# Kernel optimization log

Hardware: AMD Instinct MI355X
Metric: run time of the kernel (lower is better)

## Reference

```python
import jax, jax.numpy as jnp
import numpy as np

D_MODEL = 512
NUM_HEADS = 8
HEAD_DIM = D_MODEL // NUM_HEADS


def setup_inputs() -> dict:
    key = jax.random.key(0)
    ks = jax.random.split(key, 12)
    B, S, D = 4, 2048, D_MODEL
    s = 1.0 / np.sqrt(D)
    return {
        "x": jax.random.normal(ks[0], (B, S, D), dtype=jnp.float32),
        "timestamps": jax.random.uniform(ks[1], (B, S), dtype=jnp.float32),
        "attention_mask": jnp.ones((B, S), dtype=jnp.int32),
        "Wq": jax.random.normal(ks[2], (D, D), dtype=jnp.float32) * s,
        "bq": jnp.zeros((D,), dtype=jnp.float32),
        "Wk": jax.random.normal(ks[3], (D, D), dtype=jnp.float32) * s,
        "bk": jnp.zeros((D,), dtype=jnp.float32),
        "Wv": jax.random.normal(ks[4], (D, D), dtype=jnp.float32) * s,
        "bv": jnp.zeros((D,), dtype=jnp.float32),
        "Wo": jax.random.normal(ks[5], (D, D), dtype=jnp.float32) * s,
        "bo": jnp.zeros((D,), dtype=jnp.float32),
        "decay_lambda": jnp.ones((NUM_HEADS,), dtype=jnp.float32),
    }


def reference(x, timestamps, attention_mask, Wq, bq, Wk, bk, Wv, bv, Wo, bo, decay_lambda):
    B, S, D = x.shape
    H, hd = NUM_HEADS, HEAD_DIM
    scale = hd ** -0.5
    q = (x @ Wq + bq).reshape(B, S, H, hd)
    k = (x @ Wk + bk).reshape(B, S, H, hd)
    v = (x @ Wv + bv).reshape(B, S, H, hd)
    # [B,H,S,S] raw scores
    scores = jnp.einsum("bihd,bjhd->bhij", q, k) * scale
    # learnable exponential time decay, multiplied into scores
    time_diff_abs = jnp.abs(timestamps[:, :, None] - timestamps[:, None, :])  # [B,S,S]
    lam = jax.nn.softplus(decay_lambda)  # [H]
    decay_bias = jnp.exp(-lam[None, :, None, None] * time_diff_abs[:, None])  # [B,H,S,S]
    scores = scores * decay_bias
    # mask over key positions
    scores = jnp.where(attention_mask[:, None, None, :] == 0, -jnp.inf, scores)
    attn = jax.nn.softmax(scores, axis=-1)
    out = jnp.einsum("bhij,bjhd->bihd", attn, v).reshape(B, S, D)
    out = out @ Wo + bo
    return out, attn
```

## Files before the change

kernel.cpp:

```cpp
#include <hip/hip_runtime.h>


#define S_LEN  2048
#define DM     512
#define NH     8
#define HDIM   64
#define BATCH  4
#define BHN    32
#define BSROWS 8192

typedef __attribute__((ext_vector_type(8))) short short8v;
typedef __attribute__((ext_vector_type(8))) unsigned short ushort8v;
typedef __attribute__((ext_vector_type(4))) unsigned short ushort4v;
typedef __attribute__((ext_vector_type(4))) float f32x4;
typedef __attribute__((ext_vector_type(2))) unsigned int uint2v;

static __device__ __forceinline__ unsigned short bf16_rne(float f){
  unsigned int u = __float_as_uint(f);
  u = (u + 0x7FFFu + ((u >> 16) & 1u)) >> 16;
  return (unsigned short)u;
}
static __device__ __forceinline__ float bf16_f32(unsigned short h){
  return __uint_as_float(((unsigned int)h) << 16);
}
static __device__ __forceinline__ unsigned int pack2bf(float a, float b){
  return (unsigned int)bf16_rne(a) | ((unsigned int)bf16_rne(b) << 16);
}
static __device__ __forceinline__ f32x4 mfma16(short8v a, short8v b, f32x4 c){
  return __builtin_amdgcn_mfma_f32_16x16x32_bf16(a, b, c, 0, 0, 0);
}
static __device__ __forceinline__ void gll16(const unsigned short* g, unsigned short* l){
  __builtin_amdgcn_global_load_lds(
      (const __attribute__((address_space(1))) unsigned int*)g,
      (__attribute__((address_space(3))) unsigned int*)l, 16, 0, 0);
}

__global__ void k_split(const float* __restrict__ src,
                        unsigned short* __restrict__ hi,
                        unsigned short* __restrict__ lo, int n){
  for (int i = blockIdx.x*blockDim.x + threadIdx.x; i < n;
       i += gridDim.x*blockDim.x){
    float f = src[i];
    unsigned short h = bf16_rne(f);
    hi[i] = h;
    lo[i] = bf16_rne(f - bf16_f32(h));
  }
}

__global__ void k_wsplit4(
    const float* __restrict__ Wq, const float* __restrict__ Wk,
    const float* __restrict__ Wv, const float* __restrict__ Wo,
    unsigned short* __restrict__ qkvh, unsigned short* __restrict__ qkvl,
    unsigned short* __restrict__ oh,   unsigned short* __restrict__ ol)
{
  int idx = blockIdx.x*blockDim.x + threadIdx.x;
  int wsel = idx >> 18;
  int off  = idx & 262143;
  int n = off >> 9, k = off & 511;
  const float* W = wsel==0 ? Wq : wsel==1 ? Wk : wsel==2 ? Wv : Wo;
  unsigned short* H = (wsel<3) ? (qkvh + (size_t)wsel*262144) : oh;
  unsigned short* L = (wsel<3) ? (qkvl + (size_t)wsel*262144) : ol;
  float f = W[k*DM + n];
  unsigned short h = bf16_rne(f);
  H[off] = h;
  L[off] = bf16_rne(f - bf16_f32(h));
}

__global__ __launch_bounds__(256, 3) void k_gemm_qkv(
    const unsigned short* __restrict__ Ahi, const unsigned short* __restrict__ Alo,
    const unsigned short* __restrict__ BThi, const unsigned short* __restrict__ BTlo,
    const float* __restrict__ bq, const float* __restrict__ bk,
    const float* __restrict__ bv,
    unsigned short* __restrict__ qhi, unsigned short* __restrict__ qlo,
    unsigned short* __restrict__ khi, unsigned short* __restrict__ klo,
    unsigned short* __restrict__ vt)
{
  const int K = DM;
  __shared__ __align__(16) unsigned short At[2][2][128][32];
  __shared__ __align__(16) unsigned short Bt[2][2][64][32];
  const int lane = threadIdx.x & 63, w = threadIdx.x >> 6;
  const int lr = lane & 15, lk = lane >> 4;
  const int rowbase = blockIdx.y*128;
  const int colbase = blockIdx.x*64;
  const int wrow = (w >> 1)*64;
  const int wcol = (w & 1)*32;

  const int srow = w*16 + (lane>>2);
  const int ssw  = ((lane&3) ^ ((lane>>3)&3))*8;
  const unsigned short* asrc_h = Ahi + (size_t)(rowbase + srow)*K + ssw;
  const unsigned short* asrc_l = Alo + (size_t)(rowbase + srow)*K + ssw;
  const unsigned short* bsrc_h = BThi + (size_t)(colbase + srow)*K + ssw;
  const unsigned short* bsrc_l = BTlo + (size_t)(colbase + srow)*K + ssw;
  unsigned short* adst_h = &At[0][0][w*16][0];
  unsigned short* adst_l = &At[0][1][w*16][0];
  unsigned short* bdst_h = &Bt[0][0][w*16][0];
  unsigned short* bdst_l = &Bt[0][1][w*16][0];

#define GSTAGE(KS, BB) { \
    int k0_ = (KS)*32; \
    gll16(asrc_h + k0_,                adst_h + (BB)*8192); \
    gll16(asrc_h + (size_t)64*K + k0_, adst_h + (BB)*8192 + 2048); \
    gll16(asrc_l + k0_,                adst_l + (BB)*8192); \
    gll16(asrc_l + (size_t)64*K + k0_, adst_l + (BB)*8192 + 2048); \
    gll16(bsrc_h + k0_,                bdst_h + (BB)*4096); \
    gll16(bsrc_l + k0_,                bdst_l + (BB)*4096); }

  const int csw = (lk ^ ((lr>>1)&3))*8;
  const unsigned short* Ard_h = &At[0][0][wrow + lr][0] + csw;
  const unsigned short* Ard_l = &At[0][1][wrow + lr][0] + csw;
  const unsigned short* Brd_h = &Bt[0][0][wcol + lr][0] + csw;
  const unsigned short* Brd_l = &Bt[0][1][wcol + lr][0] + csw;

  f32x4 acc[4][2];
#pragma unroll
  for (int mi=0; mi<4; ++mi)
#pragma unroll
    for (int ni=0; ni<2; ++ni) acc[mi][ni] = (f32x4){0.f,0.f,0.f,0.f};

  GSTAGE(0, 0);
  __syncthreads();

  const int NKS = K >> 5;
  for (int ks = 0; ks < NKS; ++ks){
    const int c = ks & 1;
    if (ks + 1 < NKS) GSTAGE(ks+1, c^1);
    short8v ah[4], al[4], bhf[2], blf[2];
#pragma unroll
    for (int mi=0; mi<4; ++mi){
      ah[mi] = *(const short8v*)(Ard_h + c*8192 + mi*512);
      al[mi] = *(const short8v*)(Ard_l + c*8192 + mi*512);
    }
#pragma unroll
    for (int ni=0; ni<2; ++ni){
      bhf[ni] = *(const short8v*)(Brd_h + c*4096 + ni*512);
      blf[ni] = *(const short8v*)(Brd_l + c*4096 + ni*512);
    }
#pragma unroll
    for (int mi=0; mi<4; ++mi)
#pragma unroll
      for (int ni=0; ni<2; ++ni){
        acc[mi][ni] = mfma16(ah[mi], blf[ni], acc[mi][ni]);
        acc[mi][ni] = mfma16(al[mi], bhf[ni], acc[mi][ni]);
        acc[mi][ni] = mfma16(ah[mi], bhf[ni], acc[mi][ni]);
      }
    __syncthreads();
  }
#undef GSTAGE

  const int seg = colbase >> 9;
#pragma unroll
  for (int mi=0; mi<4; ++mi)
#pragma unroll
    for (int ni=0; ni<2; ++ni){
      const int col = colbase + wcol + ni*16 + lr;
      const int c2  = col & 511;
      const int row0 = rowbase + wrow + mi*16 + lk*4;
      const int b = row0 >> 11, s0 = row0 & 2047, hh = c2 >> 6, d = c2 & 63;
      if (seg == 2){
        float bias = bv[c2];
        ushort4v t;
#pragma unroll
        for (int r=0;r<4;++r) t[r] = bf16_rne(acc[mi][ni][r] + bias);
        *(ushort4v*)(vt + ((size_t)(b*NH + hh)*HDIM + d)*S_LEN + s0) = t;
      } else {
        const float bias = seg ? bk[c2] : bq[c2];
        const float scl  = seg ? 1.f : 0.18033688f;
        unsigned short* oh = seg ? khi : qhi;
        unsigned short* ol = seg ? klo : qlo;
#pragma unroll
        for (int r=0;r<4;++r){
          float cvl = (acc[mi][ni][r] + bias) * scl;
          size_t off = (((size_t)(b*NH + hh))*S_LEN + s0 + r)*HDIM + d;
          unsigned short hb = bf16_rne(cvl);
          oh[off] = hb;
          ol[off] = bf16_rne(cvl - bf16_f32(hb));
        }
      }
    }
}

__global__ __launch_bounds__(256, 3) void k_gemm_out(
    const unsigned short* __restrict__ Ahi, const unsigned short* __restrict__ Alo,
    const unsigned short* __restrict__ BThi, const unsigned short* __restrict__ BTlo,
    const float* __restrict__ bias, float* __restrict__ outF)
{
  const int K = DM, N = DM;
  __shared__ __align__(16) unsigned short At[2][2][128][32];
  __shared__ __align__(16) unsigned short Bt[2][2][64][32];
  const int lane = threadIdx.x & 63, w = threadIdx.x >> 6;
  const int lr = lane & 15, lk = lane >> 4;
  const int rowbase = blockIdx.y*128;
  const int colbase = blockIdx.x*64;
  const int wrow = (w >> 1)*64;
  const int wcol = (w & 1)*32;

  const int srow = w*16 + (lane>>2);
  const int ssw  = ((lane&3) ^ ((lane>>3)&3))*8;
  const unsigned short* asrc_h = Ahi + (size_t)(rowbase + srow)*K + ssw;
  const unsigned short* asrc_l = Alo + (size_t)(rowbase + srow)*K + ssw;
  const unsigned short* bsrc_h = BThi + (size_t)(colbase + srow)*K + ssw;
  const unsigned short* bsrc_l = BTlo + (size_t)(colbase + srow)*K + ssw;
  unsigned short* adst_h = &At[0][0][w*16][0];
  unsigned short* adst_l = &At[0][1][w*16][0];
  unsigned short* bdst_h = &Bt[0][0][w*16][0];
  unsigned short* bdst_l = &Bt[0][1][w*16][0];

#define GSTAGE(KS, BB) { \
    int k0_ = (KS)*32; \
    gll16(asrc_h + k0_,                adst_h + (BB)*8192); \
    gll16(asrc_h + (size_t)64*K + k0_, adst_h + (BB)*8192 + 2048); \
    gll16(asrc_l + k0_,                adst_l + (BB)*8192); \
    gll16(asrc_l + (size_t)64*K + k0_, adst_l + (BB)*8192 + 2048); \
    gll16(bsrc_h + k0_,                bdst_h + (BB)*4096); \
    gll16(bsrc_l + k0_,                bdst_l + (BB)*4096); }

  const int csw = (lk ^ ((lr>>1)&3))*8;
  const unsigned short* Ard_h = &At[0][0][wrow + lr][0] + csw;
  const unsigned short* Ard_l = &At[0][1][wrow + lr][0] + csw;
  const unsigned short* Brd_h = &Bt[0][0][wcol + lr][0] + csw;
  const unsigned short* Brd_l = &Bt[0][1][wcol + lr][0] + csw;

  f32x4 acc[4][2];
#pragma unroll
  for (int mi=0; mi<4; ++mi)
#pragma unroll
    for (int ni=0; ni<2; ++ni) acc[mi][ni] = (f32x4){0.f,0.f,0.f,0.f};

  GSTAGE(0, 0);
  __syncthreads();

  const int NKS = K >> 5;
  for (int ks = 0; ks < NKS; ++ks){
    const int c = ks & 1;
    if (ks + 1 < NKS) GSTAGE(ks+1, c^1);
    short8v ah[4], al[4], bhf[2], blf[2];
#pragma unroll
    for (int mi=0; mi<4; ++mi){
      ah[mi] = *(const short8v*)(Ard_h + c*8192 + mi*512);
      al[mi] = *(const short8v*)(Ard_l + c*8192 + mi*512);
    }
#pragma unroll
    for (int ni=0; ni<2; ++ni){
      bhf[ni] = *(const short8v*)(Brd_h + c*4096 + ni*512);
      blf[ni] = *(const short8v*)(Brd_l + c*4096 + ni*512);
    }
#pragma unroll
    for (int mi=0; mi<4; ++mi)
#pragma unroll
      for (int ni=0; ni<2; ++ni){
        acc[mi][ni] = mfma16(ah[mi], blf[ni], acc[mi][ni]);
        acc[mi][ni] = mfma16(al[mi], bhf[ni], acc[mi][ni]);
        acc[mi][ni] = mfma16(ah[mi], bhf[ni], acc[mi][ni]);
      }
    __syncthreads();
  }
#undef GSTAGE

#pragma unroll
  for (int mi=0; mi<4; ++mi)
#pragma unroll
    for (int ni=0; ni<2; ++ni){
      const int col = colbase + wcol + ni*16 + lr;
      const int row0 = rowbase + wrow + mi*16 + lk*4;
#pragma unroll
      for (int r=0;r<4;++r)
        outF[(size_t)(row0 + r)*N + col] = acc[mi][ni][r] + bias[col];
    }
}

__global__ __launch_bounds__(256) void k_rowsum(
    const unsigned short* __restrict__ qhi,
    const unsigned short* __restrict__ khi,
    const float* __restrict__ ts, const int* __restrict__ am,
    const float* __restrict__ dlam,
    float* __restrict__ rs_part)
{
  __shared__ __align__(16) unsigned short K_t[2][32][64];
  __shared__ __align__(16) float ts_l[1024];
  __shared__ __align__(16) float mb_l[1024];
  const int w = threadIdx.x >> 6, lane = threadIdx.x & 63;
  const int lr = lane & 15, lk = lane >> 4;
  const int wg = blockIdx.x;
  const int sw = (wg & 7)*256 + (wg >> 3);
  const int bh = sw >> 6, rem = sw & 63, it = rem >> 1, jh = rem & 1;
  const int b = bh >> 3, h = bh & 7;
  const int i0 = it*64 + w*16;
  const int j0 = jh*1024;

  const float* tsb = ts + b*S_LEN;
  const int*   amb = am + b*S_LEN;
  for (int i = threadIdx.x; i < 1024; i += 256){
    ts_l[i] = tsb[j0+i];
    mb_l[i] = amb[j0+i] ? 0.f : -1e30f;
  }

  float nlam2 = -log1pf(expf(dlam[h])) * 1.44269504f;
  nlam2 = __uint_as_float(__builtin_amdgcn_readfirstlane(__float_as_uint(nlam2)));

  size_t qoff = ((size_t)bh*S_LEN + i0 + lr)*HDIM + lk*8;
  const short8v qh0 = *(const short8v*)(qhi + qoff);
  const short8v qh1 = *(const short8v*)(qhi + qoff + 32);
  const float ti = tsb[i0 + lr];

  const unsigned short* kbh = khi + ((size_t)bh*S_LEN + j0)*HDIM;
  const unsigned short* ksrc = kbh + ((lane>>3))*64
                             + (((lane&7)^((lane>>3)&7))*8) + w*512;
  unsigned short* kdst = &K_t[0][0][0] + w*512;

  gll16(ksrc, kdst);
  __syncthreads();

  float rs = 0.f;
  for (int t = 0; t < 32; ++t){
    const int c = t & 1;
    if (t < 31) gll16(ksrc + (t+1)*2048, kdst + (c^1)*2048);
#pragma unroll
    for (int s = 0; s < 2; ++s){
      const unsigned short* Kr = &K_t[c][s*16 + lr][0];
      short8v a0 = *(const short8v*)(Kr + ((lk ^ (lr&7))*8));
      short8v a1 = *(const short8v*)(Kr + (((4+lk) ^ (lr&7))*8));
      f32x4 sA = (f32x4){0.f,0.f,0.f,0.f};
      sA = mfma16(a0, qh0, sA);
      sA = mfma16(a1, qh1, sA);
      const int jb = t*32 + s*16 + lk*4;
      f32x4 ts4 = *(const f32x4*)&ts_l[jb];
      f32x4 mb4 = *(const f32x4*)&mb_l[jb];
#pragma unroll
      for (int r=0;r<4;++r){
        float dec = __builtin_amdgcn_exp2f(nlam2 * fabsf(ti - ts4[r]));
        rs += __builtin_amdgcn_exp2f(__builtin_fmaf(sA[r], dec, mb4[r]));
      }
    }
    __syncthreads();
  }
  rs += __shfl_xor(rs, 16, 64);
  rs += __shfl_xor(rs, 32, 64);
  if (lane < 16)
    rs_part[(size_t)(jh*BHN + bh)*S_LEN + i0 + lane] = rs;
}

__global__ __launch_bounds__(256, 4) void k_pass2(
    const unsigned short* __restrict__ qhi, const unsigned short* __restrict__ qlo,
    const unsigned short* __restrict__ khi, const unsigned short* __restrict__ klo,
    const unsigned short* __restrict__ vT,
    const float* __restrict__ ts, const int* __restrict__ am,
    const float* __restrict__ dlam,
    const float* __restrict__ rs_part,
    float* __restrict__ attn,
    unsigned short* __restrict__ p0hi, unsigned short* __restrict__ p0lo,
    unsigned short* __restrict__ p1hi, unsigned short* __restrict__ p1lo)
{
  __shared__ __align__(16) unsigned short K_t[2][2][32][64];
  __shared__ __align__(16) unsigned short V_t[2][64][32];
  __shared__ __align__(16) float ts_l[1024];
  __shared__ __align__(16) float mb_l[1024];
  __shared__ __align__(16) unsigned int pb[4][16][20];
  const int w = threadIdx.x >> 6, lane = threadIdx.x & 63;
  const int lr = lane & 15, lk = lane >> 4;
  const int wg = blockIdx.x;
  const int sw = (wg & 7)*256 + (wg >> 3);
  const int bh = sw >> 6, rem = sw & 63, it = rem >> 1, jh = rem & 1;
  const int b = bh >> 3, h = bh & 7;
  const int i0 = it*64 + w*16;
  const int j0 = jh*1024;

  const float* tsb = ts + b*S_LEN;
  const int*   amb = am + b*S_LEN;
  for (int i = threadIdx.x; i < 1024; i += 256){
    ts_l[i] = tsb[j0+i];
    mb_l[i] = amb[j0+i] ? 0.f : -1e30f;
  }

  float nlam2 = -log1pf(expf(dlam[h])) * 1.44269504f;
  nlam2 = __uint_as_float(__builtin_amdgcn_readfirstlane(__float_as_uint(nlam2)));

  size_t qoff = ((size_t)bh*S_LEN + i0 + lr)*HDIM + lk*8;
  const short8v qh0 = *(const short8v*)(qhi + qoff);
  const short8v qh1 = *(const short8v*)(qhi + qoff + 32);
  const short8v ql0 = *(const short8v*)(qlo + qoff);
  const short8v ql1 = *(const short8v*)(qlo + qoff + 32);
  const float ti = tsb[i0 + lr];

  float tot = rs_part[(size_t)bh*S_LEN + i0 + lr]
            + rs_part[(size_t)(BHN + bh)*S_LEN + i0 + lr];
  const float rinv = tot > 0.f ? 1.f/tot : 0.f;

  const unsigned short* kbh = khi + ((size_t)bh*S_LEN + j0)*HDIM;
  const unsigned short* kbl = klo + ((size_t)bh*S_LEN + j0)*HDIM;
  const unsigned short* vtb = vT + (size_t)bh*HDIM*S_LEN;
  unsigned int* pbw = &pb[w][0][0];

  const int ksw = ((lane&7)^((lane>>3)&7))*8;
  const unsigned short* ksrc_h = kbh + (lane>>3)*64 + ksw + w*512;
  const unsigned short* ksrc_l = kbl + (lane>>3)*64 + ksw + w*512;
  const unsigned short* vsrc = vtb + ((size_t)(w*16 + (lane>>2)))*S_LEN + j0
                             + (((lane&3)^((lane>>4)&3))*8);
  unsigned short* kdst_h = &K_t[0][0][0][0] + w*512;
  unsigned short* kdst_l = &K_t[0][1][0][0] + w*512;
  unsigned short* vdst   = &V_t[0][0][0]    + w*512;

  const unsigned int abase = (unsigned int)(bh*S_LEN + i0 + lr)*S_LEN + j0;

  gll16(ksrc_h, kdst_h);
  gll16(ksrc_l, kdst_l);
  gll16(vsrc,   vdst);
  __syncthreads();

  f32x4 oaccT0 = (f32x4){0.f,0.f,0.f,0.f};
  f32x4 oaccT1 = (f32x4){0.f,0.f,0.f,0.f};
  f32x4 oaccT2 = (f32x4){0.f,0.f,0.f,0.f};
  f32x4 oaccT3 = (f32x4){0.f,0.f,0.f,0.f};

  for (int t = 0; t < 32; ++t){
    const int c = t & 1;
    if (t < 31){
      gll16(ksrc_h + (t+1)*2048, kdst_h + (c^1)*4096);
      gll16(ksrc_l + (t+1)*2048, kdst_l + (c^1)*4096);
      gll16(vsrc   + (t+1)*32,   vdst   + (c^1)*2048);
    }
#pragma unroll
    for (int s = 0; s < 2; ++s){
      const unsigned short* Kr0 = &K_t[c][0][s*16 + lr][0];
      const unsigned short* Kr1 = &K_t[c][1][s*16 + lr][0];
      short8v kh0 = *(const short8v*)(Kr0 + ((lk ^ (lr&7))*8));
      short8v kh1 = *(const short8v*)(Kr0 + (((4+lk) ^ (lr&7))*8));
      short8v kl0 = *(const short8v*)(Kr1 + ((lk ^ (lr&7))*8));
      short8v kl1 = *(const short8v*)(Kr1 + (((4+lk) ^ (lr&7))*8));
      f32x4 s1 = (f32x4){0.f,0.f,0.f,0.f};
      s1 = mfma16(kh0, ql0, s1);
      s1 = mfma16(kl0, qh0, s1);
      s1 = mfma16(kh1, ql1, s1);
      s1 = mfma16(kl1, qh1, s1);
      f32x4 s2 = (f32x4){0.f,0.f,0.f,0.f};
      s2 = mfma16(kh0, qh0, s2);
      s2 = mfma16(kh1, qh1, s2);
      const int jb = t*32 + s*16 + lk*4;
      f32x4 ts4 = *(const f32x4*)&ts_l[jb];
      f32x4 mb4 = *(const f32x4*)&mb_l[jb];
      f32x4 pv;
#pragma unroll
      for (int r=0;r<4;++r){
        float sa = s1[r] + s2[r];
        float dec = __builtin_amdgcn_exp2f(nlam2 * fabsf(ti - ts4[r]));
        float e = __builtin_amdgcn_exp2f(__builtin_fmaf(sa, dec, mb4[r]));
        pv[r] = e * rinv;
      }
      *(f32x4*)(attn + abase + jb) = pv;
      uint2v pk; pk.x = pack2bf(pv[0], pv[1]); pk.y = pack2bf(pv[2], pv[3]);
      *(uint2v*)&pbw[lr*20 + s*8 + 2*lk] = pk;
    }
    short8v pa = *(const short8v*)&pbw[lr*20 + 4*lk];
    const int vsw = (lr>>2)&3;
    short8v vf0 = *(const short8v*)&V_t[c][ 0 + lr][(lk ^ vsw)*8];
    short8v vf1 = *(const short8v*)&V_t[c][16 + lr][(lk ^ vsw)*8];
    short8v vf2 = *(const short8v*)&V_t[c][32 + lr][(lk ^ vsw)*8];
    short8v vf3 = *(const short8v*)&V_t[c][48 + lr][(lk ^ vsw)*8];
    oaccT0 = mfma16(vf0, pa, oaccT0);
    oaccT1 = mfma16(vf1, pa, oaccT1);
    oaccT2 = mfma16(vf2, pa, oaccT2);
    oaccT3 = mfma16(vf3, pa, oaccT3);
    asm volatile("s_waitcnt vmcnt(2) lgkmcnt(0)" ::: "memory");
    __builtin_amdgcn_s_barrier();
  }

  unsigned short* phi = jh ? p1hi : p0hi;
  unsigned short* plo = jh ? p1lo : p0lo;
  const size_t rowb = (size_t)(b*S_LEN + i0 + lr)*DM + h*HDIM + lk*4;
  float oa[4][4] = {
    {oaccT0[0],oaccT0[1],oaccT0[2],oaccT0[3]},
    {oaccT1[0],oaccT1[1],oaccT1[2],oaccT1[3]},
    {oaccT2[0],oaccT2[1],oaccT2[2],oaccT2[3]},
    {oaccT3[0],oaccT3[1],oaccT3[2],oaccT3[3]}};
#pragma unroll
  for (int nt=0;nt<4;++nt){
    ushort4v hh, ll;
#pragma unroll
    for (int r=0;r<4;++r){
      float vv = oa[nt][r];
      unsigned short hb = bf16_rne(vv);
      hh[r] = hb;
      ll[r] = bf16_rne(vv - bf16_f32(hb));
    }
    *(ushort4v*)(phi + rowb + nt*16) = hh;
    *(ushort4v*)(plo + rowb + nt*16) = ll;
  }
}

__global__ __launch_bounds__(256) void k_combine(
    const unsigned short* __restrict__ h1, const unsigned short* __restrict__ l1,
    unsigned short* __restrict__ oh, unsigned short* __restrict__ ol, int n8)
{
  int i = blockIdx.x*blockDim.x + threadIdx.x;
  if (i >= n8) return;
  size_t base = (size_t)i*8;
  ushort8v a = *(const ushort8v*)(oh + base);
  ushort8v bq = *(const ushort8v*)(ol + base);
  ushort8v c = *(const ushort8v*)(h1 + base);
  ushort8v d = *(const ushort8v*)(l1 + base);
  ushort8v rh, rl;
#pragma unroll
  for (int j=0;j<8;++j){
    float f = bf16_f32(a[j]) + bf16_f32(bq[j]) + bf16_f32(c[j]) + bf16_f32(d[j]);
    unsigned short hb = bf16_rne(f);
    rh[j] = hb;
    rl[j] = bf16_rne(f - bf16_f32(hb));
  }
  *(ushort8v*)(oh + base) = rh;
  *(ushort8v*)(ol + base) = rl;
}

extern "C" void kernel_launch(void* const* d_in, const int* in_sizes, int n_in,
                              void* d_out, int out_size, void* d_ws, size_t ws_size,
                              hipStream_t stream){
  const float* x  = (const float*)d_in[0];
  const float* ts = (const float*)d_in[1];
  const int*   am = (const int*)d_in[2];
  const float* Wq = (const float*)d_in[3];
  const float* bq = (const float*)d_in[4];
  const float* Wk = (const float*)d_in[5];
  const float* bk = (const float*)d_in[6];
  const float* Wv = (const float*)d_in[7];
  const float* bv = (const float*)d_in[8];
  const float* Wo = (const float*)d_in[9];
  const float* bo = (const float*)d_in[10];
  const float* dl = (const float*)d_in[11];

  char* ws = (char*)d_ws;
  unsigned short* xhi = (unsigned short*)(ws);
  unsigned short* xlo = (unsigned short*)(ws + 8388608ull);
  unsigned short* wqkv_hi = (unsigned short*)(ws + 16777216ull);
  unsigned short* wqkv_lo = (unsigned short*)(ws + 16777216ull + 1572864ull);
  unsigned short* wot_hi  = (unsigned short*)(ws + 16777216ull + 3145728ull);
  unsigned short* wot_lo  = (unsigned short*)(ws + 16777216ull + 3670016ull);
  unsigned short* qhi = (unsigned short*)(ws + 20971520ull + 0ull*8388608ull);
  unsigned short* qlo = (unsigned short*)(ws + 20971520ull + 1ull*8388608ull);
  unsigned short* khi = (unsigned short*)(ws + 20971520ull + 2ull*8388608ull);
  unsigned short* klo = (unsigned short*)(ws + 20971520ull + 3ull*8388608ull);
  unsigned short* vt  = (unsigned short*)(ws + 20971520ull + 4ull*8388608ull);
  float* rs_part = (float*)(ws + 16777216ull);

  float* outp  = (float*)d_out;
  float* attnp = outp + (size_t)BSROWS*DM;
  unsigned short* p1hi = (unsigned short*)d_out;
  unsigned short* p1lo = p1hi + 4194304ull;

  k_split<<<4096, 256, 0, stream>>>(x, xhi, xlo, BSROWS*DM);
  k_wsplit4<<<4096, 256, 0, stream>>>(Wq, Wk, Wv, Wo,
                                      wqkv_hi, wqkv_lo, wot_hi, wot_lo);

  k_gemm_qkv<<<dim3(1536/64, BSROWS/128), 256, 0, stream>>>(
      xhi, xlo, wqkv_hi, wqkv_lo, bq, bk, bv, qhi, qlo, khi, klo, vt);

  k_rowsum<<<2048, 256, 0, stream>>>(qhi, khi, ts, am, dl, rs_part);
  k_pass2<<<2048, 256, 0, stream>>>(qhi, qlo, khi, klo, vt, ts, am, dl,
                                    rs_part, attnp, xhi, xlo, p1hi, p1lo);
  k_combine<<<2048, 256, 0, stream>>>(p1hi, p1lo, xhi, xlo, 524288);
  k_gemm_out<<<dim3(DM/64, BSROWS/128), 256, 0, stream>>>(
      xhi, xlo, wot_hi, wot_lo, bo, outp);

  (void)in_sizes; (void)n_in; (void)out_size; (void)ws_size;
}
```

Measured before the change: 373.7 us.

## Double pass2 block rows to share K/V tiles; tile-transpose weight split

k_pass2 now uses 512-thread blocks covering 128 query rows instead of 64. Each K/V tile staged in LDS is therefore reused by eight waves, which halves global K/V traffic per query row. The staging work is split so waves 0-3 load K hi/lo and waves 4-7 load V. Separately, the weight split/transpose kernel now transposes through an LDS tile with vectorized loads and stores instead of strided scalar reads. The risks are lower occupancy per block under launch_bounds(512,4) register pressure, and a pass2 grid with half as many blocks.

Measured after the change: 358.0 us. -4.2%, faster.

```diff
diff --git a/kernel.cpp b/kernel.cpp
--- a/kernel.cpp
+++ b/kernel.cpp
@@ -47,23 +47,42 @@
   }
 }
 
-__global__ void k_wsplit4(
+__global__ __launch_bounds__(256) void k_wsplit4(
     const float* __restrict__ Wq, const float* __restrict__ Wk,
     const float* __restrict__ Wv, const float* __restrict__ Wo,
     unsigned short* __restrict__ qkvh, unsigned short* __restrict__ qkvl,
     unsigned short* __restrict__ oh,   unsigned short* __restrict__ ol)
 {
-  int idx = blockIdx.x*blockDim.x + threadIdx.x;
-  int wsel = idx >> 18;
-  int off  = idx & 262143;
-  int n = off >> 9, k = off & 511;
+  __shared__ __align__(16) float tile[64][68];
+  const int bid = blockIdx.x;
+  const int wsel = bid >> 6;
+  const int tk = (bid >> 3) & 7, tn = bid & 7;
   const float* W = wsel==0 ? Wq : wsel==1 ? Wk : wsel==2 ? Wv : Wo;
   unsigned short* H = (wsel<3) ? (qkvh + (size_t)wsel*262144) : oh;
   unsigned short* L = (wsel<3) ? (qkvl + (size_t)wsel*262144) : ol;
-  float f = W[k*DM + n];
-  unsigned short h = bf16_rne(f);
-  H[off] = h;
-  L[off] = bf16_rne(f - bf16_f32(h));
+  const int k0 = tk*64, n0 = tn*64;
+  const int rr = threadIdx.x >> 2, seg = threadIdx.x & 3;
+
+  const float* src = W + (size_t)(k0 + rr)*DM + n0 + seg*16;
+  *(f32x4*)&tile[rr][seg*16 + 0]  = *(const f32x4*)(src + 0);
+  *(f32x4*)&tile[rr][seg*16 + 4]  = *(const f32x4*)(src + 4);
+  *(f32x4*)&tile[rr][seg*16 + 8]  = *(const f32x4*)(src + 8);
+  *(f32x4*)&tile[rr][seg*16 + 12] = *(const f32x4*)(src + 12);
+  __syncthreads();
+
+  ushort8v h0, h1, l0, l1;
+#pragma unroll
+  for (int i=0;i<16;++i){
+    float f = tile[seg*16 + i][rr];
+    unsigned short hb = bf16_rne(f);
+    unsigned short lb = bf16_rne(f - bf16_f32(hb));
+    if (i < 8){ h0[i] = hb; l0[i] = lb; } else { h1[i-8] = hb; l1[i-8] = lb; }
+  }
+  size_t off = (size_t)(n0 + rr)*DM + k0 + seg*16;
+  *(ushort8v*)(H + off)     = h0;
+  *(ushort8v*)(H + off + 8) = h1;
+  *(ushort8v*)(L + off)     = l0;
+  *(ushort8v*)(L + off + 8) = l1;
 }
 
 __global__ __launch_bounds__(256, 3) void k_gemm_qkv(
@@ -339,7 +358,7 @@
     rs_part[(size_t)(jh*BHN + bh)*S_LEN + i0 + lane] = rs;
 }
 
-__global__ __launch_bounds__(256, 4) void k_pass2(
+__global__ __launch_bounds__(512, 4) void k_pass2(
     const unsigned short* __restrict__ qhi, const unsigned short* __restrict__ qlo,
     const unsigned short* __restrict__ khi, const unsigned short* __restrict__ klo,
     const unsigned short* __restrict__ vT,
@@ -354,19 +373,19 @@
   __shared__ __align__(16) unsigned short V_t[2][64][32];
   __shared__ __align__(16) float ts_l[1024];
   __shared__ __align__(16) float mb_l[1024];
-  __shared__ __align__(16) unsigned int pb[4][16][20];
+  __shared__ __align__(16) unsigned int pb[8][16][20];
   const int w = threadIdx.x >> 6, lane = threadIdx.x & 63;
   const int lr = lane & 15, lk = lane >> 4;
   const int wg = blockIdx.x;
-  const int sw = (wg & 7)*256 + (wg >> 3);
-  const int bh = sw >> 6, rem = sw & 63, it = rem >> 1, jh = rem & 1;
+  const int sw = (wg & 7)*128 + (wg >> 3);
+  const int bh = sw >> 5, rem = sw & 31, it = rem >> 1, jh = rem & 1;
   const int b = bh >> 3, h = bh & 7;
-  const int i0 = it*64 + w*16;
+  const int i0 = it*128 + w*16;
   const int j0 = jh*1024;
 
   const float* tsb = ts + b*S_LEN;
   const int*   amb = am + b*S_LEN;
-  for (int i = threadIdx.x; i < 1024; i += 256){
+  for (int i = threadIdx.x; i < 1024; i += 512){
     ts_l[i] = tsb[j0+i];
     mb_l[i] = amb[j0+i] ? 0.f : -1e30f;
   }
@@ -391,19 +410,22 @@
   unsigned int* pbw = &pb[w][0][0];
 
   const int ksw = ((lane&7)^((lane>>3)&7))*8;
-  const unsigned short* ksrc_h = kbh + (lane>>3)*64 + ksw + w*512;
-  const unsigned short* ksrc_l = kbl + (lane>>3)*64 + ksw + w*512;
-  const unsigned short* vsrc = vtb + ((size_t)(w*16 + (lane>>2)))*S_LEN + j0
+  const unsigned short* ksrc_h = kbh + (lane>>3)*64 + ksw + (w&3)*512;
+  const unsigned short* ksrc_l = kbl + (lane>>3)*64 + ksw + (w&3)*512;
+  const unsigned short* vsrc = vtb + ((size_t)((w&3)*16 + (lane>>2)))*S_LEN + j0
                              + (((lane&3)^((lane>>4)&3))*8);
-  unsigned short* kdst_h = &K_t[0][0][0][0] + w*512;
-  unsigned short* kdst_l = &K_t[0][1][0][0] + w*512;
-  unsigned short* vdst   = &V_t[0][0][0]    + w*512;
+  unsigned short* kdst_h = &K_t[0][0][0][0] + (w&3)*512;
+  unsigned short* kdst_l = &K_t[0][1][0][0] + (w&3)*512;
+  unsigned short* vdst   = &V_t[0][0][0]    + (w&3)*512;
 
   const unsigned int abase = (unsigned int)(bh*S_LEN + i0 + lr)*S_LEN + j0;
 
-  gll16(ksrc_h, kdst_h);
-  gll16(ksrc_l, kdst_l);
-  gll16(vsrc,   vdst);
+  if (w < 4){
+    gll16(ksrc_h, kdst_h);
+    gll16(ksrc_l, kdst_l);
+  } else {
+    gll16(vsrc, vdst);
+  }
   __syncthreads();
 
   f32x4 oaccT0 = (f32x4){0.f,0.f,0.f,0.f};
@@ -414,9 +436,12 @@
   for (int t = 0; t < 32; ++t){
     const int c = t & 1;
     if (t < 31){
-      gll16(ksrc_h + (t+1)*2048, kdst_h + (c^1)*4096);
-      gll16(ksrc_l + (t+1)*2048, kdst_l + (c^1)*4096);
-      gll16(vsrc   + (t+1)*32,   vdst   + (c^1)*2048);
+      if (w < 4){
+        gll16(ksrc_h + (t+1)*2048, kdst_h + (c^1)*4096);
+        gll16(ksrc_l + (t+1)*2048, kdst_l + (c^1)*4096);
+      } else {
+        gll16(vsrc + (t+1)*32, vdst + (c^1)*2048);
+      }
     }
 #pragma unroll
     for (int s = 0; s < 2; ++s){
@@ -545,14 +570,14 @@
   unsigned short* p1lo = p1hi + 4194304ull;
 
   k_split<<<4096, 256, 0, stream>>>(x, xhi, xlo, BSROWS*DM);
-  k_wsplit4<<<4096, 256, 0, stream>>>(Wq, Wk, Wv, Wo,
-                                      wqkv_hi, wqkv_lo, wot_hi, wot_lo);
+  k_wsplit4<<<256, 256, 0, stream>>>(Wq, Wk, Wv, Wo,
+                                     wqkv_hi, wqkv_lo, wot_hi, wot_lo);
 
   k_gemm_qkv<<<dim3(1536/64, BSROWS/128), 256, 0, stream>>>(
       xhi, xlo, wqkv_hi, wqkv_lo, bq, bk, bv, qhi, qlo, khi, klo, vt);
 
   k_rowsum<<<2048, 256, 0, stream>>>(qhi, khi, ts, am, dl, rs_part);
-  k_pass2<<<2048, 256, 0, stream>>>(qhi, qlo, khi, klo, vt, ts, am, dl,
+  k_pass2<<<1024, 512, 0, stream>>>(qhi, qlo, khi, klo, vt, ts, am, dl,
                                     rs_part, attnp, xhi, xlo, p1hi, p1lo);
   k_combine<<<2048, 256, 0, stream>>>(p1hi, p1lo, xhi, xlo, 524288);
   k_gemm_out<<<dim3(DM/64, BSROWS/128), 256, 0, stream>>>(
```
